# Kernel tuning notes

Hardware: AMD Instinct MI355X
Metric: run time of the kernel (lower is better)

The kernel has to match this reference:

```python
import jax, jax.numpy as jnp
import numpy as np

N_SOTU, N_TAXON = 100000, 20000
E, EL = 800000, 200000
D_S, D_T, H = 256, 128, 256


def setup_inputs() -> dict:
    key = jax.random.key(0)
    ks = jax.random.split(key, 32)
    nrm = lambda k, shp: jax.random.normal(k, shp, jnp.float32) * 0.05
    inp = {}
    inp["x_sotu"] = nrm(ks[0], (N_SOTU, D_S))
    inp["x_taxon"] = nrm(ks[1], (N_TAXON, D_T))
    inp["edge_src"] = jax.random.randint(ks[2], (E,), 0, N_SOTU)   # sotu end
    inp["edge_dst"] = jax.random.randint(ks[3], (E,), 0, N_TAXON)  # taxon end
    inp["label_src"] = jax.random.randint(ks[4], (EL,), 0, N_SOTU)
    inp["label_dst"] = jax.random.randint(ks[5], (EL,), 0, N_TAXON)
    # conv1, edge type sotu->taxon
    inp["Wl1_st"] = nrm(ks[6], (H, D_S)); inp["bl1_st"] = jnp.zeros((H,), jnp.float32)
    inp["Wr1_st"] = nrm(ks[7], (H, D_T))
    # conv1, edge type taxon->sotu (reverse)
    inp["Wl1_ts"] = nrm(ks[8], (H, D_T)); inp["bl1_ts"] = jnp.zeros((H,), jnp.float32)
    inp["Wr1_ts"] = nrm(ks[9], (H, D_S))
    # conv2 (hidden -> hidden) per edge type
    inp["Wl2_st"] = nrm(ks[10], (H, H)); inp["bl2_st"] = jnp.zeros((H,), jnp.float32)
    inp["Wr2_st"] = nrm(ks[11], (H, H))
    inp["Wl2_ts"] = nrm(ks[12], (H, H)); inp["bl2_ts"] = jnp.zeros((H,), jnp.float32)
    inp["Wr2_ts"] = nrm(ks[13], (H, H))
    # final per-node-type linear (to_hetero duplicates Linear per node type)
    inp["Wlin_s"] = nrm(ks[14], (H, H)); inp["blin_s"] = jnp.zeros((H,), jnp.float32)
    inp["Wlin_t"] = nrm(ks[15], (H, H)); inp["blin_t"] = jnp.zeros((H,), jnp.float32)
    # edge decoder MLP
    inp["Wd1"] = nrm(ks[16], (H, 2 * H)); inp["bd1"] = jnp.zeros((H,), jnp.float32)
    inp["Wd2"] = nrm(ks[17], (1, H));     inp["bd2"] = jnp.zeros((1,), jnp.float32)
    return inp


def _sage(x_src, x_dst, src, dst, Wl, bl, Wr):
    """PyG SAGEConv (mean aggr): lin_l(mean of neighbor src feats) + lin_r(x_dst)."""
    n_dst = x_dst.shape[0]
    msum = jax.ops.segment_sum(x_src[src], dst, num_segments=n_dst)
    cnt = jax.ops.segment_sum(jnp.ones(src.shape, x_src.dtype), dst, num_segments=n_dst)
    m = msum / jnp.maximum(cnt, 1.0)[:, None]
    return m @ Wl.T + bl + x_dst @ Wr.T


def reference(x_sotu, x_taxon, edge_src, edge_dst, label_src, label_dst,
              Wl1_st, bl1_st, Wr1_st, Wl1_ts, bl1_ts, Wr1_ts,
              Wl2_st, bl2_st, Wr2_st, Wl2_ts, bl2_ts, Wr2_ts,
              Wlin_s, blin_s, Wlin_t, blin_t, Wd1, bd1, Wd2, bd2):
    # layer 1 (hetero SAGE, aggr='sum' over single incoming edge type per node type)
    h1_t = jax.nn.relu(_sage(x_sotu, x_taxon, edge_src, edge_dst, Wl1_st, bl1_st, Wr1_st))
    h1_s = jax.nn.relu(_sage(x_taxon, x_sotu, edge_dst, edge_src, Wl1_ts, bl1_ts, Wr1_ts))
    # layer 2
    h2_t = jax.nn.relu(_sage(h1_s, h1_t, edge_src, edge_dst, Wl2_st, bl2_st, Wr2_st))
    h2_s = jax.nn.relu(_sage(h1_t, h1_s, edge_dst, edge_src, Wl2_ts, bl2_ts, Wr2_ts))
    # per-node-type output projection
    z_s = h2_s @ Wlin_s.T + blin_s
    z_t = h2_t @ Wlin_t.T + blin_t
    # edge decoder: gather endpoint embeddings, concat, 2-layer MLP
    z = jnp.concatenate([z_s[label_src], z_t[label_dst]], axis=-1)  # [EL, 2H]
    h = jax.nn.relu(z @ Wd1.T + bd1)
    return (h @ Wd2.T + bd2).reshape(-1)  # [EL]
```

## Files before the change

kernel.cpp:

```cpp
#include <hip/hip_runtime.h>


constexpr int NS = 100000, NT = 20000;
constexpr int E_EDGES = 800000, EL_EDGES = 200000;
constexpr int DS = 256, DT = 128, H = 256;

constexpr int NB_T = 79, SH_T = 8, VB_T = 17;
constexpr int NB_S = 98, SH_S = 10, VB_S = 15;
constexpr int BIN_CAP = 96, CHUNK = 2048;
constexpr int CVT_BLOCKS = 2048;

typedef __attribute__((ext_vector_type(8))) short short8;
typedef __attribute__((ext_vector_type(4))) float float4v;
typedef __attribute__((ext_vector_type(8))) _Float16 half8v;
typedef unsigned short ushort_t;

__device__ __forceinline__ float bf2f(unsigned int u) {
    union { unsigned int i; float f; } x; x.i = u << 16; return x.f;
}
__device__ __forceinline__ unsigned short f2bf(float f) {
    union { float f; unsigned int i; } x; x.f = f;
    unsigned int r = x.i + 0x7FFFu + ((x.i >> 16) & 1u);
    return (unsigned short)(r >> 16);
}


struct GemmJob {
    const ushort_t* A1; const ushort_t* W1; int K1;
    const ushort_t* A2; const ushort_t* W2; int K2;
    const ushort_t* Add; const float* bias;
    void* C; int M; int flags;
};

struct GatherJob {
    const ushort_t* X; const int* rowptr; const int* cnt; const int* col;
    ushort_t* out; int N;
};

struct Gather128Job {
    const ushort_t* X; const int* rowptr; const int* cnt; const int* col;
    ushort_t* out; int N;
};

__device__ __forceinline__ void gemm_body(const GemmJob& jb, int bid)
{
    __shared__ ushort_t As[64][40];
    __shared__ ushort_t Bs[128][40];
    const int tid = threadIdx.x;
    const int M = jb.M;

    const int nx = (M + 63) >> 6;
    const int nx8 = nx & ~7;
    int rowblk, colblk;
    if (bid < nx8 * 2) {
        const int group = bid >> 4;
        const int xcd = bid & 7;
        const int half = (bid >> 3) & 1;
        rowblk = group * 8 + xcd;
        colblk = half;
    } else {
        const int r = bid - nx8 * 2;
        rowblk = nx8 + (r >> 1);
        colblk = r & 1;
    }
    const int row0 = rowblk * 64, col0 = colblk * 128;

    const int wave = tid >> 6, lane = tid & 63;
    const int wrow = (wave >> 1) * 32;
    const int wcol = (wave & 1) * 64;
    const int m16 = lane & 15, quad = lane >> 4;
    const int sr = tid >> 2;
    const int skc = (tid & 3) * 8;

    float4v acc[2][4];
#pragma unroll
    for (int i = 0; i < 2; i++)
#pragma unroll
        for (int j = 0; j < 4; j++) acc[i][j] = (float4v){0.f, 0.f, 0.f, 0.f};

#pragma unroll 1
    for (int pass = 0; pass < 2; pass++) {
        const ushort_t* A = pass ? jb.A2 : jb.A1;
        const ushort_t* W = pass ? jb.W2 : jb.W1;
        const int K = pass ? jb.K2 : jb.K1;
        if (!A) break;
        const int gra = row0 + sr;
        const bool oka = gra < M;
        const ushort_t* Ap = A + (size_t)gra * K + skc;
        const ushort_t* Wp0 = W + (size_t)(col0 + sr) * K + skc;
        const ushort_t* Wp1 = W + (size_t)(col0 + 64 + sr) * K + skc;

        uint4 a0 = make_uint4(0, 0, 0, 0);
        if (oka) a0 = *(const uint4*)Ap;
        uint4 b0 = *(const uint4*)Wp0;
        uint4 b1 = *(const uint4*)Wp1;

        for (int k0 = 0; k0 < K; k0 += 32) {
            __syncthreads();
            *(uint4*)&As[sr][skc] = a0;
            *(uint4*)&Bs[sr][skc] = b0;
            *(uint4*)&Bs[64 + sr][skc] = b1;
            __syncthreads();
            if (k0 + 32 < K) {
                a0 = make_uint4(0, 0, 0, 0);
                if (oka) a0 = *(const uint4*)(Ap + k0 + 32);
                b0 = *(const uint4*)(Wp0 + k0 + 32);
                b1 = *(const uint4*)(Wp1 + k0 + 32);
            }
            short8 af[2], bf[4];
#pragma unroll
            for (int i = 0; i < 2; i++)
                af[i] = *(const short8*)&As[wrow + i * 16 + m16 - wrow][quad * 8 + (wrow ? 0 : 0)];
#pragma unroll
            for (int i = 0; i < 2; i++)
                af[i] = *(const short8*)&As[wrow + i * 16 + m16 - (wrow ? wrow : 0) + (wrow ? wrow : 0) - wrow + wrow][quad * 8];
#pragma unroll
            for (int i = 0; i < 2; i++)
                af[i] = *(const short8*)&As[wrow + i * 16 + m16][quad * 8];
#pragma unroll
            for (int j = 0; j < 4; j++)
                bf[j] = *(const short8*)&Bs[wcol + j * 16 + m16][quad * 8];
#pragma unroll
            for (int i = 0; i < 2; i++)
#pragma unroll
                for (int j = 0; j < 4; j++)
                    acc[i][j] = __builtin_amdgcn_mfma_f32_16x16x32_bf16(
                        af[i], bf[j], acc[i][j], 0, 0, 0);
        }
    }

    const bool relu = jb.flags & 1, f16out = jb.flags & 2;
#pragma unroll
    for (int i = 0; i < 2; i++) {
        const int rbase = row0 + wrow + i * 16 + quad * 4;
#pragma unroll
        for (int r = 0; r < 4; r++) {
            const int row = rbase + r;
            if (row >= M) continue;
#pragma unroll
            for (int j = 0; j < 4; j++) {
                const int col = col0 + wcol + j * 16 + m16;
                float v = acc[i][j][r];
                if (jb.Add) v += bf2f((unsigned int)jb.Add[(size_t)row * 256 + col]);
                if (jb.bias) v += jb.bias[col];
                if (relu) v = fmaxf(v, 0.f);
                if (f16out) ((_Float16*)jb.C)[(size_t)row * 256 + col] = (_Float16)v;
                else ((ushort_t*)jb.C)[(size_t)row * 256 + col] = f2bf(v);
            }
        }
    }
}

#define UNPACK_ADD(acc, v) \
    acc[0] += bf2f(v.x & 0xffff); acc[1] += bf2f(v.x >> 16); \
    acc[2] += bf2f(v.y & 0xffff); acc[3] += bf2f(v.y >> 16); \
    acc[4] += bf2f(v.z & 0xffff); acc[5] += bf2f(v.z >> 16); \
    acc[6] += bf2f(v.w & 0xffff); acc[7] += bf2f(v.w >> 16);

__device__ __forceinline__ void gather_body(const GatherJob& g, int gb)
{
    const int node = gb * 16 + (threadIdx.x >> 5);
    const int c = (threadIdx.x & 31) * 8;
    if (node >= g.N) return;
    const int beg = g.rowptr[node];
    const int deg = g.cnt[node];
    const int end = beg + deg;
    const ushort_t* __restrict__ X = g.X;
    const int* __restrict__ col = g.col;
    float a[8] = {0, 0, 0, 0, 0, 0, 0, 0};
    float b[8] = {0, 0, 0, 0, 0, 0, 0, 0};
    int i = beg;
    for (; i + 3 < end; i += 4) {
        const int c0 = col[i], c1 = col[i + 1], c2 = col[i + 2], c3 = col[i + 3];
        uint4 v0 = *(const uint4*)&X[(size_t)c0 * 256 + c];
        uint4 v1 = *(const uint4*)&X[(size_t)c1 * 256 + c];
        uint4 v2 = *(const uint4*)&X[(size_t)c2 * 256 + c];
        uint4 v3 = *(const uint4*)&X[(size_t)c3 * 256 + c];
        UNPACK_ADD(a, v0) UNPACK_ADD(b, v1) UNPACK_ADD(a, v2) UNPACK_ADD(b, v3)
    }
    for (; i + 1 < end; i += 2) {
        uint4 v0 = *(const uint4*)&X[(size_t)col[i] * 256 + c];
        uint4 v1 = *(const uint4*)&X[(size_t)col[i + 1] * 256 + c];
        UNPACK_ADD(a, v0) UNPACK_ADD(b, v1)
    }
    if (i < end) {
        uint4 v0 = *(const uint4*)&X[(size_t)col[i] * 256 + c];
        UNPACK_ADD(a, v0)
    }
    float inv = 1.f / fmaxf((float)deg, 1.f);
    uint4 o;
    o.x = (unsigned int)f2bf((a[0] + b[0]) * inv) | ((unsigned int)f2bf((a[1] + b[1]) * inv) << 16);
    o.y = (unsigned int)f2bf((a[2] + b[2]) * inv) | ((unsigned int)f2bf((a[3] + b[3]) * inv) << 16);
    o.z = (unsigned int)f2bf((a[4] + b[4]) * inv) | ((unsigned int)f2bf((a[5] + b[5]) * inv) << 16);
    o.w = (unsigned int)f2bf((a[6] + b[6]) * inv) | ((unsigned int)f2bf((a[7] + b[7]) * inv) << 16);
    *(uint4*)&g.out[(size_t)node * 256 + c] = o;
}

__device__ __forceinline__ void gather128_body(const Gather128Job& g, int gb)
{
    const int node = gb * 32 + (threadIdx.x >> 4);
    const int c = (threadIdx.x & 15) * 8;
    if (node >= g.N) return;
    const int beg = g.rowptr[node];
    const int deg = g.cnt[node];
    const int end = beg + deg;
    const ushort_t* __restrict__ X = g.X;
    const int* __restrict__ col = g.col;
    float a[8] = {0, 0, 0, 0, 0, 0, 0, 0};
    float b[8] = {0, 0, 0, 0, 0, 0, 0, 0};
    int i = beg;
    for (; i + 3 < end; i += 4) {
        const int c0 = col[i], c1 = col[i + 1], c2 = col[i + 2], c3 = col[i + 3];
        uint4 v0 = *(const uint4*)&X[(size_t)c0 * 128 + c];
        uint4 v1 = *(const uint4*)&X[(size_t)c1 * 128 + c];
        uint4 v2 = *(const uint4*)&X[(size_t)c2 * 128 + c];
        uint4 v3 = *(const uint4*)&X[(size_t)c3 * 128 + c];
        UNPACK_ADD(a, v0) UNPACK_ADD(b, v1) UNPACK_ADD(a, v2) UNPACK_ADD(b, v3)
    }
    for (; i + 1 < end; i += 2) {
        uint4 v0 = *(const uint4*)&X[(size_t)col[i] * 128 + c];
        uint4 v1 = *(const uint4*)&X[(size_t)col[i + 1] * 128 + c];
        UNPACK_ADD(a, v0) UNPACK_ADD(b, v1)
    }
    if (i < end) {
        uint4 v0 = *(const uint4*)&X[(size_t)col[i] * 128 + c];
        UNPACK_ADD(a, v0)
    }
    float inv = 1.f / fmaxf((float)deg, 1.f);
    uint4 o;
    o.x = (unsigned int)f2bf((a[0] + b[0]) * inv) | ((unsigned int)f2bf((a[1] + b[1]) * inv) << 16);
    o.y = (unsigned int)f2bf((a[2] + b[2]) * inv) | ((unsigned int)f2bf((a[3] + b[3]) * inv) << 16);
    o.z = (unsigned int)f2bf((a[4] + b[4]) * inv) | ((unsigned int)f2bf((a[5] + b[5]) * inv) << 16);
    o.w = (unsigned int)f2bf((a[6] + b[6]) * inv) | ((unsigned int)f2bf((a[7] + b[7]) * inv) << 16);
    *(uint4*)&g.out[(size_t)node * 128 + c] = o;
}

__global__ __launch_bounds__(256) void gemm_gemm_kernel(GemmJob a, int ablocks,
                                                        GemmJob b)
{
    const int bid = blockIdx.x;
    if (bid < ablocks) gemm_body(a, bid);
    else gemm_body(b, bid - ablocks);
}

__global__ __launch_bounds__(512) void gather_g128_kernel(GatherJob a, int ablocks,
                                                          Gather128Job b)
{
    const int bid = blockIdx.x;
    if (bid < ablocks) gather_body(a, bid);
    else gather128_body(b, bid - ablocks);
}

__global__ __launch_bounds__(512) void gather_gather_kernel(GatherJob a, int ablocks,
                                                            GatherJob b)
{
    const int bid = blockIdx.x;
    if (bid < ablocks) gather_body(a, bid);
    else gather_body(b, bid - ablocks);
}

struct CvtJobs {
    const float* src[14];
    ushort_t* dst[14];
    int n4[14];
    int cnt;
};

__global__ __launch_bounds__(256) void cvt_kernel(CvtJobs jb, int nchunks)
{
    const int t = threadIdx.x;
#pragma unroll 1
    for (int ch = blockIdx.x; ch < nchunks; ch += gridDim.x) {
        int idx = ch << 10;
        int k = 0;
        while (idx >= jb.n4[k]) { idx -= jb.n4[k]; ++k; }
        const float4* __restrict__ s = (const float4*)jb.src[k];
        ushort_t* __restrict__ d = jb.dst[k];
        const int base = idx + t;
        float4 v0 = s[base];
        float4 v1 = s[base + 256];
        float4 v2 = s[base + 512];
        float4 v3 = s[base + 768];
        uint2 o0, o1, o2, o3;
        o0.x = (unsigned int)f2bf(v0.x) | ((unsigned int)f2bf(v0.y) << 16);
        o0.y = (unsigned int)f2bf(v0.z) | ((unsigned int)f2bf(v0.w) << 16);
        o1.x = (unsigned int)f2bf(v1.x) | ((unsigned int)f2bf(v1.y) << 16);
        o1.y = (unsigned int)f2bf(v1.z) | ((unsigned int)f2bf(v1.w) << 16);
        o2.x = (unsigned int)f2bf(v2.x) | ((unsigned int)f2bf(v2.y) << 16);
        o2.y = (unsigned int)f2bf(v2.z) | ((unsigned int)f2bf(v2.w) << 16);
        o3.x = (unsigned int)f2bf(v3.x) | ((unsigned int)f2bf(v3.y) << 16);
        o3.y = (unsigned int)f2bf(v3.z) | ((unsigned int)f2bf(v3.w) << 16);
        *(uint2*)(d + (size_t)base * 4) = o0;
        *(uint2*)(d + (size_t)(base + 256) * 4) = o1;
        *(uint2*)(d + (size_t)(base + 512) * 4) = o2;
        *(uint2*)(d + (size_t)(base + 768) * 4) = o3;
    }
}

__global__ __launch_bounds__(256) void count_kernel(
    const int* __restrict__ src, const int* __restrict__ dst,
    int* __restrict__ cnt_s, int* __restrict__ cnt_t, int E)
{
    const int base = blockIdx.x * 1024 + threadIdx.x;
    const int e0 = base, e1 = base + 256, e2 = base + 512, e3 = base + 768;
    int s0 = 0, s1 = 0, s2 = 0, s3 = 0;
    int d0 = 0, d1 = 0, d2 = 0, d3 = 0;
    if (e0 < E) { s0 = src[e0]; d0 = dst[e0]; }
    if (e1 < E) { s1 = src[e1]; d1 = dst[e1]; }
    if (e2 < E) { s2 = src[e2]; d2 = dst[e2]; }
    if (e3 < E) { s3 = src[e3]; d3 = dst[e3]; }
    if (e0 < E) { atomicAdd(&cnt_s[s0], 1); atomicAdd(&cnt_t[d0], 1); }
    if (e1 < E) { atomicAdd(&cnt_s[s1], 1); atomicAdd(&cnt_t[d1], 1); }
    if (e2 < E) { atomicAdd(&cnt_s[s2], 1); atomicAdd(&cnt_t[d2], 1); }
    if (e3 < E) { atomicAdd(&cnt_s[s3], 1); atomicAdd(&cnt_t[d3], 1); }
}

__global__ __launch_bounds__(256) void fold_kernel(
    const float* __restrict__ Wd1, const float* __restrict__ bd1,
    const float* __restrict__ Wlin_s, const float* __restrict__ blin_s,
    const float* __restrict__ Wlin_t, const float* __restrict__ blin_t,
    float* __restrict__ Wc_s, float* __restrict__ Wc_t,
    float* __restrict__ bu, float* __restrict__ bv)
{
    const int b = blockIdx.x, t = threadIdx.x;
    if (b < 256) {
        float s = 0.f;
        for (int k = 0; k < 256; k++) s += Wd1[b * 512 + k] * Wlin_s[k * 256 + t];
        Wc_s[b * 256 + t] = s;
    } else if (b < 512) {
        const int h = b - 256;
        float s = 0.f;
        for (int k = 0; k < 256; k++) s += Wd1[h * 512 + 256 + k] * Wlin_t[k * 256 + t];
        Wc_t[h * 256 + t] = s;
    } else {
        float su = 0.f, sv = 0.f;
        for (int k = 0; k < 256; k++) {
            su += Wd1[t * 512 + k] * blin_s[k];
            sv += Wd1[t * 512 + 256 + k] * blin_t[k];
        }
        bu[t] = bd1[t] + su;
        bv[t] = sv;
    }
}

__global__ __launch_bounds__(256) void psum_kernel(
    const int* __restrict__ cnt_s, const int* __restrict__ cnt_t,
    int* __restrict__ bsum_s, int* __restrict__ bsum_t, int nbS)
{
    const bool isS = (int)blockIdx.x < nbS;
    const int blk = isS ? blockIdx.x : blockIdx.x - nbS;
    const int N = isS ? NS : NT;
    const int* cnt = isS ? cnt_s : cnt_t;
    int* bsum = isS ? bsum_s : bsum_t;
    __shared__ int sdata[256];
    const int t = threadIdx.x;
    const int base = blk * 1024;
    int s = 0;
    for (int i = t; i < 1024; i += 256) {
        int idx = base + i;
        s += (idx < N) ? cnt[idx] : 0;
    }
    sdata[t] = s; __syncthreads();
    for (int off = 128; off > 0; off >>= 1) {
        if (t < off) sdata[t] += sdata[t + off];
        __syncthreads();
    }
    if (t == 0) bsum[blk] = sdata[0];
}

__global__ void sbsum_kernel(int* __restrict__ bsum_s, int* __restrict__ bsum_t,
                             int nbS, int nbT)
{
    if (threadIdx.x != 0) return;
    int* b = blockIdx.x ? bsum_t : bsum_s;
    int nb = blockIdx.x ? nbT : nbS;
    int run = 0;
    for (int i = 0; i < nb; i++) { int v = b[i]; b[i] = run; run += v; }
}

__global__ __launch_bounds__(256) void sblock_kernel(
    const int* __restrict__ cnt_s, const int* __restrict__ cnt_t,
    const int* __restrict__ bsum_s, const int* __restrict__ bsum_t,
    int* __restrict__ rowptr_s, int* __restrict__ rowptr_t, int nbS)
{
    const bool isS = (int)blockIdx.x < nbS;
    const int blk = isS ? blockIdx.x : blockIdx.x - nbS;
    const int N = isS ? NS : NT;
    const int* cnt = isS ? cnt_s : cnt_t;
    const int* bsum = isS ? bsum_s : bsum_t;
    int* rowptr = isS ? rowptr_s : rowptr_t;
    __shared__ int sc[256];
    const int t = threadIdx.x;
    const int base = blk * 1024 + t * 4;
    int v[4]; int s = 0;
#pragma unroll
    for (int j = 0; j < 4; j++) {
        int idx = base + j;
        v[j] = (idx < N) ? cnt[idx] : 0;
        s += v[j];
    }
    sc[t] = s; __syncthreads();
    for (int off = 1; off < 256; off <<= 1) {
        int add = (t >= off) ? sc[t - off] : 0;
        __syncthreads();
        sc[t] += add;
        __syncthreads();
    }
    int excl = sc[t] - s + bsum[blk];
#pragma unroll
    for (int j = 0; j < 4; j++) {
        int idx = base + j;
        if (idx < N) rowptr[idx] = excl;
        if (idx == N - 1) rowptr[N] = excl + v[j];
        excl += v[j];
    }
}

__global__ void binit_kernel(const int* __restrict__ rowptr_t,
                             const int* __restrict__ rowptr_s,
                             int* __restrict__ gcur_t, int* __restrict__ gcur_s)
{
    int t = threadIdx.x;
    if (t < NB_T) gcur_t[t] = rowptr_t[t << SH_T];
    if (t < NB_S) gcur_s[t] = rowptr_s[t << SH_S];
}

__global__ __launch_bounds__(256) void binA_kernel(
    const int* __restrict__ key, const int* __restrict__ val, int E,
    int nbins, int shift, int vbits,
    int* __restrict__ gcur, unsigned* __restrict__ stg)
{
    __shared__ unsigned bins[NB_S * BIN_CAP];
    __shared__ int lcnt[NB_S], gbase[NB_S];
    const int tid = threadIdx.x;
    const int base = blockIdx.x * CHUNK;
    for (int i = tid; i < nbins; i += 256) lcnt[i] = 0;
    __syncthreads();
    const unsigned lowmask = (1u << shift) - 1u;
#pragma unroll
    for (int k = 0; k < CHUNK / 256; k++) {
        int e = base + k * 256 + tid;
        if (e < E) {
            int kk = key[e];
            int b = kk >> shift;
            unsigned pk = (((unsigned)kk & lowmask) << vbits) | (unsigned)val[e];
            int c = atomicAdd(&lcnt[b], 1);
            if (c < BIN_CAP) bins[b * BIN_CAP + c] = pk;
            else { int p = atomicAdd(&gcur[b], 1); stg[p] = pk; }
        }
    }
    __syncthreads();
    if (tid < nbins) gbase[tid] = atomicAdd(&gcur[tid], min(lcnt[tid], BIN_CAP));
    __syncthreads();
    for (int b = 0; b < nbins; b++) {
        int c = min(lcnt[b], BIN_CAP);
        for (int i = tid; i < c; i += 256) stg[gbase[b] + i] = bins[b * BIN_CAP + i];
    }
}

__global__ __launch_bounds__(256) void binB_kernel(
    const unsigned* __restrict__ stg, const int* __restrict__ rowptr,
    int N, int node_per, int vbits, int* __restrict__ colout)
{
    __shared__ int cur[1024];
    const int tid = threadIdx.x;
    const int node0 = blockIdx.x * node_per;
    const int nn = min(node_per, N - node0);
    for (int i = tid; i < nn; i += 256) cur[i] = rowptr[node0 + i];
    const int estart = rowptr[node0];
    const int eend = rowptr[node0 + nn];
    __syncthreads();
    const unsigned vmask = (1u << vbits) - 1u;
    for (int i = estart + tid; i < eend; i += 256) {
        unsigned v = stg[i];
        int kl = (int)(v >> vbits);
        int pos = atomicAdd(&cur[kl], 1);
        colout[pos] = (int)(v & vmask);
    }
}

__global__ __launch_bounds__(256) void edge_score_kernel(
    const _Float16* __restrict__ U, const _Float16* __restrict__ V,
    const int* __restrict__ ls, const int* __restrict__ ld,
    const float* __restrict__ Wd2, const float* __restrict__ bd2,
    float* __restrict__ out, int EL)
{
    const int l32 = threadIdx.x & 31;
    const int e = blockIdx.x * 8 + (threadIdx.x >> 5);
    if (e >= EL) return;
    const int c = l32 * 8;
    half8v u = *(const half8v*)&U[(size_t)ls[e] * 256 + c];
    half8v v = *(const half8v*)&V[(size_t)ld[e] * 256 + c];
    float4 w0 = *(const float4*)&Wd2[c];
    float4 w1 = *(const float4*)&Wd2[c + 4];
    float s = fmaxf((float)u[0] + (float)v[0], 0.f) * w0.x
            + fmaxf((float)u[1] + (float)v[1], 0.f) * w0.y
            + fmaxf((float)u[2] + (float)v[2], 0.f) * w0.z
            + fmaxf((float)u[3] + (float)v[3], 0.f) * w0.w
            + fmaxf((float)u[4] + (float)v[4], 0.f) * w1.x
            + fmaxf((float)u[5] + (float)v[5], 0.f) * w1.y
            + fmaxf((float)u[6] + (float)v[6], 0.f) * w1.z
            + fmaxf((float)u[7] + (float)v[7], 0.f) * w1.w;
#pragma unroll
    for (int m = 16; m >= 1; m >>= 1) s += __shfl_xor(s, m, 64);
    if (l32 == 0) out[e] = s + bd2[0];
}

extern "C" void kernel_launch(void* const* d_in, const int* in_sizes, int n_in,
                              void* d_out, int out_size, void* d_ws, size_t ws_size,
                              hipStream_t stream)
{
    const float* x_sotu  = (const float*)d_in[0];
    const float* x_taxon = (const float*)d_in[1];
    const int* edge_src  = (const int*)d_in[2];
    const int* edge_dst  = (const int*)d_in[3];
    const int* label_src = (const int*)d_in[4];
    const int* label_dst = (const int*)d_in[5];
    const float* Wl1_st = (const float*)d_in[6];
    const float* bl1_st = (const float*)d_in[7];
    const float* Wr1_st = (const float*)d_in[8];
    const float* Wl1_ts = (const float*)d_in[9];
    const float* bl1_ts = (const float*)d_in[10];
    const float* Wr1_ts = (const float*)d_in[11];
    const float* Wl2_st = (const float*)d_in[12];
    const float* bl2_st = (const float*)d_in[13];
    const float* Wr2_st = (const float*)d_in[14];
    const float* Wl2_ts = (const float*)d_in[15];
    const float* bl2_ts = (const float*)d_in[16];
    const float* Wr2_ts = (const float*)d_in[17];
    const float* Wlin_s = (const float*)d_in[18];
    const float* blin_s = (const float*)d_in[19];
    const float* Wlin_t = (const float*)d_in[20];
    const float* blin_t = (const float*)d_in[21];
    const float* Wd1 = (const float*)d_in[22];
    const float* bd1 = (const float*)d_in[23];
    const float* Wd2 = (const float*)d_in[24];
    const float* bd2 = (const float*)d_in[25];

    int* wi = (int*)d_ws;
    size_t io = 0;
    int* cnt_s   = wi + io; io += NS;
    int* cnt_t   = wi + io; io += NT;
    int* rowptr_s = wi + io; io += NS + 8;
    int* rowptr_t = wi + io; io += NT + 8;
    int* col_s   = wi + io; io += E_EDGES;
    int* col_t   = wi + io; io += E_EDGES;
    unsigned* stg_s = (unsigned*)(wi + io); io += E_EDGES;
    unsigned* stg_t = (unsigned*)(wi + io); io += E_EDGES;
    int* bsum_s  = wi + io; io += 128;
    int* bsum_t  = wi + io; io += 128;
    int* gcur_t  = wi + io; io += 128;
    int* gcur_s  = wi + io; io += 128;
    io = (io + 63) & ~(size_t)63;

    ushort_t* wb = (ushort_t*)(wi + io);
    size_t bo = 0;
    ushort_t* m_s  = wb + bo; bo += (size_t)NS * H;
    ushort_t* h1_s = wb + bo; bo += (size_t)NS * H;
    ushort_t* m_t  = wb + bo; bo += (size_t)NT * H;
    ushort_t* h1_t = wb + bo; bo += (size_t)NT * H;
    ushort_t* h2_s = wb + bo; bo += (size_t)NS * H;
    ushort_t* h2_t = wb + bo; bo += (size_t)NT * H;
    ushort_t* xs_b = wb + bo; bo += (size_t)NS * DS;
    ushort_t* xt_b = wb + bo; bo += (size_t)NT * DT;
    ushort_t* wb_l1st = wb + bo; bo += H * DS;
    ushort_t* wb_r1st = wb + bo; bo += H * DT;
    ushort_t* wb_l1ts = wb + bo; bo += H * DT;
    ushort_t* wb_r1ts = wb + bo; bo += H * DS;
    ushort_t* wb_l2st = wb + bo; bo += H * H;
    ushort_t* wb_r2st = wb + bo; bo += H * H;
    ushort_t* wb_l2ts = wb + bo; bo += H * H;
    ushort_t* wb_r2ts = wb + bo; bo += H * H;
    ushort_t* wcb_s   = wb + bo; bo += H * H;
    ushort_t* wcb_t   = wb + bo; bo += H * H;
    bo = (bo + 7) & ~(size_t)7;

    float* wf = (float*)(wb + bo);
    size_t fo = 0;
    float* Wc_s = wf + fo; fo += H * H;
    float* Wc_t = wf + fo; fo += H * H;
    float* bu   = wf + fo; fo += 256;
    float* bv   = wf + fo; fo += 256;

    _Float16* U = (_Float16*)m_s;
    _Float16* V = (_Float16*)m_t;

    const dim3 blk(256);
    const dim3 blk512(512);
    auto mgn = [](int M) { return ((M + 63) / 64) * 2; };
    auto g256n = [](int N) { return (N + 15) / 16; };
    auto g128n = [](int N) { return (N + 31) / 32; };
    const int nbS = (NS + 1023) / 1024;
    const int nbT = (NT + 1023) / 1024;
    const int nA = (E_EDGES + CHUNK - 1) / CHUNK;

    fold_kernel<<<513, blk, 0, stream>>>(Wd1, bd1, Wlin_s, blin_s, Wlin_t, blin_t,
                                         Wc_s, Wc_t, bu, bv);

    hipMemsetAsync(cnt_s, 0, (size_t)(NS + NT) * sizeof(int), stream);
    count_kernel<<<(E_EDGES + 1023) / 1024, blk, 0, stream>>>(
        edge_src, edge_dst, cnt_s, cnt_t, E_EDGES);

    {
        CvtJobs jb; int c = 0, total4 = 0;
        auto addj = [&](const float* s, ushort_t* d, int n) {
            jb.src[c] = s; jb.dst[c] = d; jb.n4[c] = n / 4; total4 += n / 4; c++;
        };
        addj(x_sotu, xs_b, NS * DS);
        addj(x_taxon, xt_b, NT * DT);
        addj(Wl1_st, wb_l1st, H * DS);
        addj(Wr1_st, wb_r1st, H * DT);
        addj(Wl1_ts, wb_l1ts, H * DT);
        addj(Wr1_ts, wb_r1ts, H * DS);
        addj(Wl2_st, wb_l2st, H * H);
        addj(Wr2_st, wb_r2st, H * H);
        addj(Wl2_ts, wb_l2ts, H * H);
        addj(Wr2_ts, wb_r2ts, H * H);
        addj(Wc_s, wcb_s, H * H);
        addj(Wc_t, wcb_t, H * H);
        jb.cnt = c;
        const int nchunks = total4 >> 10;
        const int cvb = nchunks < CVT_BLOCKS ? nchunks : CVT_BLOCKS;
        cvt_kernel<<<cvb, blk, 0, stream>>>(jb, nchunks);
    }

    psum_kernel<<<nbS + nbT, blk, 0, stream>>>(cnt_s, cnt_t, bsum_s, bsum_t, nbS);
    sbsum_kernel<<<2, 64, 0, stream>>>(bsum_s, bsum_t, nbS, nbT);
    sblock_kernel<<<nbS + nbT, blk, 0, stream>>>(cnt_s, cnt_t, bsum_s, bsum_t,
                                                 rowptr_s, rowptr_t, nbS);
    binit_kernel<<<1, blk, 0, stream>>>(rowptr_t, rowptr_s, gcur_t, gcur_s);
    binA_kernel<<<nA, blk, 0, stream>>>(edge_dst, edge_src, E_EDGES,
                                        NB_T, SH_T, VB_T, gcur_t, stg_t);
    binA_kernel<<<nA, blk, 0, stream>>>(edge_src, edge_dst, E_EDGES,
                                        NB_S, SH_S, VB_S, gcur_s, stg_s);
    binB_kernel<<<NB_T, blk, 0, stream>>>(stg_t, rowptr_t, NT, 1 << SH_T, VB_T, col_t);
    binB_kernel<<<NB_S, blk, 0, stream>>>(stg_s, rowptr_s, NS, 1 << SH_S, VB_S, col_s);

    {
        GatherJob a{xs_b, rowptr_t, cnt_t, col_t, m_t, NT};
        Gather128Job b{xt_b, rowptr_s, cnt_s, col_s, m_s, NS};
        const int ab = g256n(NT);
        gather_g128_kernel<<<ab + g128n(NS), blk512, 0, stream>>>(a, ab, b);
    }
    {
        GemmJob a{xs_b, wb_r1ts, DS, m_s, wb_l1ts, DT, nullptr, bl1_ts, h1_s, NS, 1};
        GemmJob b{m_t, wb_l1st, H, xt_b, wb_r1st, DT, nullptr, bl1_st, h1_t, NT, 1};
        const int ab = mgn(NS);
        gemm_gemm_kernel<<<ab + mgn(NT), blk, 0, stream>>>(a, ab, b);
    }

    {
        GatherJob a{h1_s, rowptr_t, cnt_t, col_t, m_t, NT};
        GatherJob b{h1_t, rowptr_s, cnt_s, col_s, m_s, NS};
        const int ab = g256n(NT);
        gather_gather_kernel<<<ab + g256n(NS), blk512, 0, stream>>>(a, ab, b);
    }
    {
        GemmJob a{h1_s, wb_r2ts, H, m_s, wb_l2ts, H, nullptr, bl2_ts, h2_s, NS, 1};
        GemmJob b{m_t, wb_l2st, H, h1_t, wb_r2st, H, nullptr, bl2_st, h2_t, NT, 1};
        const int ab = mgn(NS);
        gemm_gemm_kernel<<<ab + mgn(NT), blk, 0, stream>>>(a, ab, b);
    }

    {
        GemmJob a{h2_s, wcb_s, H, nullptr, nullptr, 0, nullptr, bu, U, NS, 2};
        GemmJob b{h2_t, wcb_t, H, nullptr, nullptr, 0, nullptr, bv, V, NT, 2};
        const int ab = mgn(NS);
        gemm_gemm_kernel<<<ab + mgn(NT), blk, 0, stream>>>(a, ab, b);
    }
    edge_score_kernel<<<(EL_EDGES + 7) / 8, blk, 0, stream>>>(
        U, V, label_src, label_dst, Wd2, bd2, (float*)d_out, EL_EDGES);
}
```

Before: 782.3 us.

## Merge independent preprocessing kernels into combined launches to overlap work

Merges fold and count into one launch, cvt (weight and feature bf16 conversion) with the taxon-side binA, and the sotu-side binA with the taxon-side binB. The prefix-sum chain is moved ahead of cvt so the binning kernels can share a launch with conversion. It also drops two redundant LDS A-fragment loads in the GEMM inner loop. The aim is fewer launches and less tail idle time between small dependent kernels. The cost is larger blocks with mixed shared-memory footprints and heterogeneous blocks within one grid.

```diff
diff --git a/kernel.cpp b/kernel.cpp
--- a/kernel.cpp
+++ b/kernel.cpp
@@ -108,12 +108,6 @@
                 b1 = *(const uint4*)(Wp1 + k0 + 32);
             }
             short8 af[2], bf[4];
-#pragma unroll
-            for (int i = 0; i < 2; i++)
-                af[i] = *(const short8*)&As[wrow + i * 16 + m16 - wrow][quad * 8 + (wrow ? 0 : 0)];
-#pragma unroll
-            for (int i = 0; i < 2; i++)
-                af[i] = *(const short8*)&As[wrow + i * 16 + m16 - (wrow ? wrow : 0) + (wrow ? wrow : 0) - wrow + wrow][quad * 8];
 #pragma unroll
             for (int i = 0; i < 2; i++)
                 af[i] = *(const short8*)&As[wrow + i * 16 + m16][quad * 8];
@@ -235,28 +229,58 @@
     *(uint4*)&g.out[(size_t)node * 128 + c] = o;
 }
 
-__global__ __launch_bounds__(256) void gemm_gemm_kernel(GemmJob a, int ablocks,
-                                                        GemmJob b)
-{
-    const int bid = blockIdx.x;
-    if (bid < ablocks) gemm_body(a, bid);
-    else gemm_body(b, bid - ablocks);
-}
-
-__global__ __launch_bounds__(512) void gather_g128_kernel(GatherJob a, int ablocks,
-                                                          Gather128Job b)
-{
-    const int bid = blockIdx.x;
-    if (bid < ablocks) gather_body(a, bid);
-    else gather128_body(b, bid - ablocks);
-}
-
-__global__ __launch_bounds__(512) void gather_gather_kernel(GatherJob a, int ablocks,
-                                                            GatherJob b)
-{
-    const int bid = blockIdx.x;
-    if (bid < ablocks) gather_body(a, bid);
-    else gather_body(b, bid - ablocks);
+__device__ __forceinline__ void binA_body(
+    const int* __restrict__ key, const int* __restrict__ val, int E,
+    int nbins, int shift, int vbits,
+    int* __restrict__ gcur, unsigned* __restrict__ stg, int ablk)
+{
+    __shared__ unsigned bins[NB_S * BIN_CAP];
+    __shared__ int lcnt[NB_S], gbase[NB_S];
+    const int tid = threadIdx.x;
+    const int base = ablk * CHUNK;
+    for (int i = tid; i < nbins; i += 256) lcnt[i] = 0;
+    __syncthreads();
+    const unsigned lowmask = (1u << shift) - 1u;
+#pragma unroll
+    for (int k = 0; k < CHUNK / 256; k++) {
+        int e = base + k * 256 + tid;
+        if (e < E) {
+            int kk = key[e];
+            int b = kk >> shift;
+            unsigned pk = (((unsigned)kk & lowmask) << vbits) | (unsigned)val[e];
+            int c = atomicAdd(&lcnt[b], 1);
+            if (c < BIN_CAP) bins[b * BIN_CAP + c] = pk;
+            else { int p = atomicAdd(&gcur[b], 1); stg[p] = pk; }
+        }
+    }
+    __syncthreads();
+    if (tid < nbins) gbase[tid] = atomicAdd(&gcur[tid], min(lcnt[tid], BIN_CAP));
+    __syncthreads();
+    for (int b = 0; b < nbins; b++) {
+        int c = min(lcnt[b], BIN_CAP);
+        for (int i = tid; i < c; i += 256) stg[gbase[b] + i] = bins[b * BIN_CAP + i];
+    }
+}
+
+__device__ __forceinline__ void binB_body(
+    const unsigned* __restrict__ stg, const int* __restrict__ rowptr,
+    int N, int node_per, int vbits, int* __restrict__ colout, int bblk)
+{
+    __shared__ int cur[1024];
+    const int tid = threadIdx.x;
+    const int node0 = bblk * node_per;
+    const int nn = min(node_per, N - node0);
+    for (int i = tid; i < nn; i += 256) cur[i] = rowptr[node0 + i];
+    const int estart = rowptr[node0];
+    const int eend = rowptr[node0 + nn];
+    __syncthreads();
+    const unsigned vmask = (1u << vbits) - 1u;
+    for (int i = estart + tid; i < eend; i += 256) {
+        unsigned v = stg[i];
+        int kl = (int)(v >> vbits);
+        int pos = atomicAdd(&cur[kl], 1);
+        colout[pos] = (int)(v & vmask);
+    }
 }
 
 struct CvtJobs {
@@ -266,11 +290,12 @@
     int cnt;
 };
 
-__global__ __launch_bounds__(256) void cvt_kernel(CvtJobs jb, int nchunks)
+__device__ __forceinline__ void cvt_body(const CvtJobs& jb, int nchunks,
+                                         int ch0, int stride)
 {
     const int t = threadIdx.x;
 #pragma unroll 1
-    for (int ch = blockIdx.x; ch < nchunks; ch += gridDim.x) {
+    for (int ch = ch0; ch < nchunks; ch += stride) {
         int idx = ch << 10;
         int k = 0;
         while (idx >= jb.n4[k]) { idx -= jb.n4[k]; ++k; }
@@ -297,32 +322,14 @@
     }
 }
 
-__global__ __launch_bounds__(256) void count_kernel(
-    const int* __restrict__ src, const int* __restrict__ dst,
-    int* __restrict__ cnt_s, int* __restrict__ cnt_t, int E)
-{
-    const int base = blockIdx.x * 1024 + threadIdx.x;
-    const int e0 = base, e1 = base + 256, e2 = base + 512, e3 = base + 768;
-    int s0 = 0, s1 = 0, s2 = 0, s3 = 0;
-    int d0 = 0, d1 = 0, d2 = 0, d3 = 0;
-    if (e0 < E) { s0 = src[e0]; d0 = dst[e0]; }
-    if (e1 < E) { s1 = src[e1]; d1 = dst[e1]; }
-    if (e2 < E) { s2 = src[e2]; d2 = dst[e2]; }
-    if (e3 < E) { s3 = src[e3]; d3 = dst[e3]; }
-    if (e0 < E) { atomicAdd(&cnt_s[s0], 1); atomicAdd(&cnt_t[d0], 1); }
-    if (e1 < E) { atomicAdd(&cnt_s[s1], 1); atomicAdd(&cnt_t[d1], 1); }
-    if (e2 < E) { atomicAdd(&cnt_s[s2], 1); atomicAdd(&cnt_t[d2], 1); }
-    if (e3 < E) { atomicAdd(&cnt_s[s3], 1); atomicAdd(&cnt_t[d3], 1); }
-}
-
-__global__ __launch_bounds__(256) void fold_kernel(
+__device__ __forceinline__ void fold_body(
     const float* __restrict__ Wd1, const float* __restrict__ bd1,
     const float* __restrict__ Wlin_s, const float* __restrict__ blin_s,
     const float* __restrict__ Wlin_t, const float* __restrict__ blin_t,
     float* __restrict__ Wc_s, float* __restrict__ Wc_t,
-    float* __restrict__ bu, float* __restrict__ bv)
-{
-    const int b = blockIdx.x, t = threadIdx.x;
+    float* __restrict__ bu, float* __restrict__ bv, int b)
+{
+    const int t = threadIdx.x;
     if (b < 256) {
         float s = 0.f;
         for (int k = 0; k < 256; k++) s += Wd1[b * 512 + k] * Wlin_s[k * 256 + t];
@@ -343,6 +350,94 @@
     }
 }
 
+__device__ __forceinline__ void count_body(
+    const int* __restrict__ src, const int* __restrict__ dst,
+    int* __restrict__ cnt_s, int* __restrict__ cnt_t, int E, int cblk)
+{
+    const int base = cblk * 1024 + threadIdx.x;
+    const int e0 = base, e1 = base + 256, e2 = base + 512, e3 = base + 768;
+    int s0 = 0, s1 = 0, s2 = 0, s3 = 0;
+    int d0 = 0, d1 = 0, d2 = 0, d3 = 0;
+    if (e0 < E) { s0 = src[e0]; d0 = dst[e0]; }
+    if (e1 < E) { s1 = src[e1]; d1 = dst[e1]; }
+    if (e2 < E) { s2 = src[e2]; d2 = dst[e2]; }
+    if (e3 < E) { s3 = src[e3]; d3 = dst[e3]; }
+    if (e0 < E) { atomicAdd(&cnt_s[s0], 1); atomicAdd(&cnt_t[d0], 1); }
+    if (e1 < E) { atomicAdd(&cnt_s[s1], 1); atomicAdd(&cnt_t[d1], 1); }
+    if (e2 < E) { atomicAdd(&cnt_s[s2], 1); atomicAdd(&cnt_t[d2], 1); }
+    if (e3 < E) { atomicAdd(&cnt_s[s3], 1); atomicAdd(&cnt_t[d3], 1); }
+}
+
+__global__ __launch_bounds__(256) void gemm_gemm_kernel(GemmJob a, int ablocks,
+                                                        GemmJob b)
+{
+    const int bid = blockIdx.x;
+    if (bid < ablocks) gemm_body(a, bid);
+    else gemm_body(b, bid - ablocks);
+}
+
+__global__ __launch_bounds__(512) void gather_g128_kernel(GatherJob a, int ablocks,
+                                                          Gather128Job b)
+{
+    const int bid = blockIdx.x;
+    if (bid < ablocks) gather_body(a, bid);
+    else gather128_body(b, bid - ablocks);
+}
+
+__global__ __launch_bounds__(512) void gather_gather_kernel(GatherJob a, int ablocks,
+                                                            GatherJob b)
+{
+    const int bid = blockIdx.x;
+    if (bid < ablocks) gather_body(a, bid);
+    else gather_body(b, bid - ablocks);
+}
+
+__global__ __launch_bounds__(256) void fold_count_kernel(
+    const float* Wd1, const float* bd1,
+    const float* Wlin_s, const float* blin_s,
+    const float* Wlin_t, const float* blin_t,
+    float* Wc_s, float* Wc_t, float* bu, float* bv,
+    const int* src, const int* dst, int* cnt_s, int* cnt_t, int E)
+{
+    const int bid = blockIdx.x;
+    if (bid < 513)
+        fold_body(Wd1, bd1, Wlin_s, blin_s, Wlin_t, blin_t, Wc_s, Wc_t, bu, bv, bid);
+    else
+        count_body(src, dst, cnt_s, cnt_t, E, bid - 513);
+}
+
+__global__ __launch_bounds__(256) void cvt_binA_kernel(
+    CvtJobs jb, int nchunks, int aBlocks,
+    const int* key, const int* val, int E, int nbins, int shift, int vbits,
+    int* gcur, unsigned* stg)
+{
+    const int bid = blockIdx.x;
+    if (bid < aBlocks)
+        binA_body(key, val, E, nbins, shift, vbits, gcur, stg, bid);
+    else
+        cvt_body(jb, nchunks, bid - aBlocks, gridDim.x - aBlocks);
+}
+
+__global__ __launch_bounds__(256) void binA_binB_kernel(
+    const int* keyA, const int* valA, int E, int nbinsA, int shiftA, int vbitsA,
+    int* gcurA, unsigned* stgA, int aBlocks,
+    const unsigned* stgB, const int* rowptrB, int NB, int nodeperB, int vbitsB,
+    int* coloutB)
+{
+    const int bid = blockIdx.x;
+    if (bid < aBlocks)
+        binA_body(keyA, valA, E, nbinsA, shiftA, vbitsA, gcurA, stgA, bid);
+    else
+        binB_body(stgB, rowptrB, NB, nodeperB, vbitsB, coloutB, bid - aBlocks);
+}
+
+__global__ __launch_bounds__(256) void binB_kernel(
+    const unsigned* __restrict__ stg, const int* __restrict__ rowptr,
+    int N, int node_per, int vbits, int* __restrict__ colout)
+{
+    binB_body(stg, rowptr, N, node_per, vbits, colout, blockIdx.x);
+}
+
 __global__ __launch_bounds__(256) void psum_kernel(
     const int* __restrict__ cnt_s, const int* __restrict__ cnt_t,
     int* __restrict__ bsum_s, int* __restrict__ bsum_t, int nbS)
@@ -423,60 +518,6 @@
     int t = threadIdx.x;
     if (t < NB_T) gcur_t[t] = rowptr_t[t << SH_T];
     if (t < NB_S) gcur_s[t] = rowptr_s[t << SH_S];
-}
-
-__global__ __launch_bounds__(256) void binA_kernel(
-    const int* __restrict__ key, const int* __restrict__ val, int E,
-    int nbins, int shift, int vbits,
-    int* __restrict__ gcur, unsigned* __restrict__ stg)
-{
-    __shared__ unsigned bins[NB_S * BIN_CAP];
-    __shared__ int lcnt[NB_S], gbase[NB_S];
-    const int tid = threadIdx.x;
-    const int base = blockIdx.x * CHUNK;
-    for (int i = tid; i < nbins; i += 256) lcnt[i] = 0;
-    __syncthreads();
-    const unsigned lowmask = (1u << shift) - 1u;
-#pragma unroll
-    for (int k = 0; k < CHUNK / 256; k++) {
-        int e = base + k * 256 + tid;
-        if (e < E) {
-            int kk = key[e];
-            int b = kk >> shift;
-            unsigned pk = (((unsigned)kk & lowmask) << vbits) | (unsigned)val[e];
-            int c = atomicAdd(&lcnt[b], 1);
-            if (c < BIN_CAP) bins[b * BIN_CAP + c] = pk;
-            else { int p = atomicAdd(&gcur[b], 1); stg[p] = pk; }
-        }
-    }
-    __syncthreads();
-    if (tid < nbins) gbase[tid] = atomicAdd(&gcur[tid], min(lcnt[tid], BIN_CAP));
-    __syncthreads();
-    for (int b = 0; b < nbins; b++) {
-        int c = min(lcnt[b], BIN_CAP);
-        for (int i = tid; i < c; i += 256) stg[gbase[b] + i] = bins[b * BIN_CAP + i];
-    }
-}
-
-__global__ __launch_bounds__(256) void binB_kernel(
-    const unsigned* __restrict__ stg, const int* __restrict__ rowptr,
-    int N, int node_per, int vbits, int* __restrict__ colout)
-{
-    __shared__ int cur[1024];
-    const int tid = threadIdx.x;
-    const int node0 = blockIdx.x * node_per;
-    const int nn = min(node_per, N - node0);
-    for (int i = tid; i < nn; i += 256) cur[i] = rowptr[node0 + i];
-    const int estart = rowptr[node0];
-    const int eend = rowptr[node0 + nn];
-    __syncthreads();
-    const unsigned vmask = (1u << vbits) - 1u;
-    for (int i = estart + tid; i < eend; i += 256) {
-        unsigned v = stg[i];
-        int kl = (int)(v >> vbits);
-        int pos = atomicAdd(&cur[kl], 1);
-        colout[pos] = (int)(v & vmask);
-    }
 }
 
 __global__ __launch_bounds__(256) void edge_score_kernel(
@@ -593,13 +634,18 @@
     const int nbS = (NS + 1023) / 1024;
     const int nbT = (NT + 1023) / 1024;
     const int nA = (E_EDGES + CHUNK - 1) / CHUNK;
-
-    fold_kernel<<<513, blk, 0, stream>>>(Wd1, bd1, Wlin_s, blin_s, Wlin_t, blin_t,
-                                         Wc_s, Wc_t, bu, bv);
+    const int cntBlocks = (E_EDGES + 1023) / 1024;
 
     hipMemsetAsync(cnt_s, 0, (size_t)(NS + NT) * sizeof(int), stream);
-    count_kernel<<<(E_EDGES + 1023) / 1024, blk, 0, stream>>>(
+    fold_count_kernel<<<513 + cntBlocks, blk, 0, stream>>>(
+        Wd1, bd1, Wlin_s, blin_s, Wlin_t, blin_t, Wc_s, Wc_t, bu, bv,
         edge_src, edge_dst, cnt_s, cnt_t, E_EDGES);
+
+    psum_kernel<<<nbS + nbT, blk, 0, stream>>>(cnt_s, cnt_t, bsum_s, bsum_t, nbS);
+    sbsum_kernel<<<2, 64, 0, stream>>>(bsum_s, bsum_t, nbS, nbT);
+    sblock_kernel<<<nbS + nbT, blk, 0, stream>>>(cnt_s, cnt_t, bsum_s, bsum_t,
+                                                 rowptr_s, rowptr_t, nbS);
+    binit_kernel<<<1, blk, 0, stream>>>(rowptr_t, rowptr_s, gcur_t, gcur_s);
 
     {
         CvtJobs jb; int c = 0, total4 = 0;
@@ -621,19 +667,15 @@
         jb.cnt = c;
         const int nchunks = total4 >> 10;
         const int cvb = nchunks < CVT_BLOCKS ? nchunks : CVT_BLOCKS;
-        cvt_kernel<<<cvb, blk, 0, stream>>>(jb, nchunks);
-    }
-
-    psum_kernel<<<nbS + nbT, blk, 0, stream>>>(cnt_s, cnt_t, bsum_s, bsum_t, nbS);
-    sbsum_kernel<<<2, 64, 0, stream>>>(bsum_s, bsum_t, nbS, nbT);
-    sblock_kernel<<<nbS + nbT, blk, 0, stream>>>(cnt_s, cnt_t, bsum_s, bsum_t,
-                                                 rowptr_s, rowptr_t, nbS);
-    binit_kernel<<<1, blk, 0, stream>>>(rowptr_t, rowptr_s, gcur_t, gcur_s);
-    binA_kernel<<<nA, blk, 0, stream>>>(edge_dst, edge_src, E_EDGES,
-                                        NB_T, SH_T, VB_T, gcur_t, stg_t);
-    binA_kernel<<<nA, blk, 0, stream>>>(edge_src, edge_dst, E_EDGES,
-                                        NB_S, SH_S, VB_S, gcur_s, stg_s);
-    binB_kernel<<<NB_T, blk, 0, stream>>>(stg_t, rowptr_t, NT, 1 << SH_T, VB_T, col_t);
+        cvt_binA_kernel<<<nA + cvb, blk, 0, stream>>>(
+            jb, nchunks, nA,
+            edge_dst, edge_src, E_EDGES, NB_T, SH_T, VB_T, gcur_t, stg_t);
+    }
+
+    binA_binB_kernel<<<nA + NB_T, blk, 0, stream>>>(
+        edge_src, edge_dst, E_EDGES, NB_S, SH_S, VB_S, gcur_s, stg_s, nA,
+        stg_t, rowptr_t, NT, 1 << SH_T, VB_T, col_t);
+
     binB_kernel<<<NB_S, blk, 0, stream>>>(stg_s, rowptr_s, NS, 1 << SH_S, VB_S, col_s);
 
     {
```

After: 744.3 us. 4.9% less time.
